# Kernel tuning notes

Measured on AMD Instinct MI355X. Metric: run time of the kernel, lower is better.

The kernel has to match this reference:

```python
import jax, jax.numpy as jnp
import numpy as np

NB_KERNEL = 16
NUM_POS_EMB = 16
DMAX = 20.0


def _grbf_encode(d):
    # d: (..., ) distances; centers 0..DMAX in NB_KERNEL steps (matches torch.arange(0, 20*(1+1/15), 20/15))
    centers = jnp.linspace(0.0, DMAX, NB_KERNEL, dtype=jnp.float32)
    return jnp.exp(-jnp.square(d[..., None] - centers))


def _positional_embeddings(d):
    # d: (..., ) float offsets
    freq = jnp.exp(jnp.arange(0, NUM_POS_EMB, 2, dtype=jnp.float32) * (-(np.log(10000.0) / NUM_POS_EMB)))
    angles = d[..., None] * freq  # (..., NUM_POS_EMB//2)
    return jnp.concatenate([jnp.cos(angles), jnp.sin(angles)], axis=-1)


def setup_inputs() -> dict:
    key = jax.random.key(0)
    # coordinates in Angstrom-ish scale so pairwise distances span the RBF range
    crd = jax.random.normal(key, (4096, 4, 3), dtype=jnp.float32) * 10.0
    return {"crd": crd, "max_neigh": 64}


def reference(crd, max_neigh):
    nb_var = crd.shape[0]
    nb_neigh = min(max_neigh, nb_var - 1)

    # virtual Cbeta atom from backbone geometry
    b = crd[:, 1] - crd[:, 0]
    c = crd[:, 2] - crd[:, 1]
    a = jnp.cross(b, c)
    Cb = -0.58273431 * a + 0.56802827 * b - 0.54067466 * c + crd[:, 1]
    crd5 = jnp.concatenate([crd, Cb[:, None, :]], axis=1)  # (N, 5, 3)

    # pairwise CA distances, diagonal forced to -1 so self sorts first
    ca = crd5[:, 1]  # (N, 3)
    D = jnp.linalg.norm(ca[:, None, :] - ca[None, :, :], axis=-1)  # (N, N)
    diag = jnp.arange(nb_var)
    D = D.at[diag, diag].set(-1.0)

    # nb_neigh smallest distances (= top_k of -D); self is column 0
    neg_d, idx_pairs = jax.lax.top_k(-D, nb_neigh)  # (N, K)
    d = -neg_d
    d = d.at[:, 0].set(0.0)
    d = jnp.nan_to_num(d, nan=0.0)

    # all-pairs atom distances between residue i (5 atoms) and each neighbor j (5 atoms)
    neigh = crd5[idx_pairs]  # (N, K, 5, 3)
    diff = crd5[:, None, :, None, :] - neigh[:, :, None, :, :]  # (N, K, 5, 5, 3); [i,k,a,b]=crd[i,a]-crd[j,b]
    dist = jnp.linalg.norm(diff, axis=-1).reshape(nb_var, nb_neigh, 25)
    dist = _grbf_encode(dist).reshape(nb_var, nb_neigh, 25 * NB_KERNEL)
    dist = jnp.nan_to_num(dist, nan=0.0)

    # sinusoidal encoding of sequence-index offsets
    offsets = jnp.abs(diag[:, None] - idx_pairs).astype(jnp.float32)  # (N, K)
    pos = _positional_embeddings(offsets)  # (N, K, NUM_POS_EMB)

    return (d, dist, pos, idx_pairs)
```

## Files before the change

### kernel.cpp

```cpp
#include <hip/hip_runtime.h>
#include <math.h>

#define NBV 4096
#define KNE 64
#define D_OFF    0
#define DIST_OFF (NBV*KNE)
#define POS_OFF  (DIST_OFF + NBV*KNE*400)
#define IDX_OFF  (POS_OFF + NBV*KNE*16)

#define WS_CRD5 0
#define WS_CA4  (NBV*16)
#define WS_FLOATS (NBV*16 + NBV*4)

typedef float f4v __attribute__((ext_vector_type(4)));

__device__ __forceinline__ unsigned int f2sort(float f) {
  unsigned int u = __float_as_uint(f);
  return (u & 0x80000000u) ? ~u : (u | 0x80000000u);
}
__device__ __forceinline__ float sort2f(unsigned int s) {
  unsigned int u = (s & 0x80000000u) ? (s & 0x7FFFFFFFu) : ~s;
  return __uint_as_float(u);
}

__device__ __forceinline__ float4 crd5_f4(const float* __restrict__ crd, int r,
                                          int q) {
  if (q < 3) return ((const float4*)crd)[r * 3 + q];
  const float4 a = ((const float4*)crd)[r * 3 + 0];
  const float4 b = ((const float4*)crd)[r * 3 + 1];
  const float4 c = ((const float4*)crd)[r * 3 + 2];
  const float bx = a.w - a.x, by = b.x - a.y, bz = b.y - a.z;
  const float cx = b.z - a.w, cy = b.w - b.x, cz = c.x - b.y;
  const float axv = by * cz - bz * cy;
  const float ayv = bz * cx - bx * cz;
  const float azv = bx * cy - by * cx;
  return make_float4(
      -0.58273431f * axv + 0.56802827f * bx - 0.54067466f * cx + a.w,
      -0.58273431f * ayv + 0.56802827f * by - 0.54067466f * cy + b.x,
      -0.58273431f * azv + 0.56802827f * bz - 0.54067466f * cz + b.y, 0.0f);
}

__global__ __launch_bounds__(256) void prep_k(const float* __restrict__ crd,
                                              float* __restrict__ ws) {
  const int r = blockIdx.x * 256 + threadIdx.x;
  const float4 a = ((const float4*)crd)[r * 3 + 0];
  const float4 b = ((const float4*)crd)[r * 3 + 1];
  const float4 c = ((const float4*)crd)[r * 3 + 2];
  const float bx = a.w - a.x, by = b.x - a.y, bz = b.y - a.z;
  const float cx = b.z - a.w, cy = b.w - b.x, cz = c.x - b.y;
  const float axv = by * cz - bz * cy;
  const float ayv = bz * cx - bx * cz;
  const float azv = bx * cy - by * cx;
  const float cbx = -0.58273431f * axv + 0.56802827f * bx - 0.54067466f * cx + a.w;
  const float cby = -0.58273431f * ayv + 0.56802827f * by - 0.54067466f * cy + b.x;
  const float cbz = -0.58273431f * azv + 0.56802827f * bz - 0.54067466f * cz + b.y;

  float4* row = (float4*)(ws + WS_CRD5 + r * 16);
  row[0] = a;
  row[1] = b;
  row[2] = c;
  row[3] = make_float4(cbx, cby, cbz, 0.0f);
  ((float4*)(ws + WS_CA4))[r] = make_float4(a.w, b.x, b.y, 0.0f);
}

template <bool USE_WS>
__global__ __launch_bounds__(256) void fused_k(const float* __restrict__ crd,
                                               const float* __restrict__ ws,
                                               float* __restrict__ out) {
  const int i = blockIdx.x;
  const int t = threadIdx.x;

  __shared__ float region0[2688];
  __shared__ unsigned long long cand[512];
  __shared__ int jidx[64];
  __shared__ unsigned int cnt;
  __shared__ int selbin;
  __shared__ unsigned int wsum[4];

  unsigned int* hist = (unsigned int*)region0;
  float* rows = region0;
  float* dvals = region0 + 1040;

  for (int b = t; b < 2048; b += 256) hist[b] = 0u;
  if (t == 0) cnt = 0u;
  __syncthreads();

  float cax, cay, caz;
  if (USE_WS) {
    const float4 c4 = ((const float4*)(ws + WS_CA4))[i];
    cax = c4.x; cay = c4.y; caz = c4.z;
  } else {
    cax = crd[i * 12 + 3]; cay = crd[i * 12 + 4]; caz = crd[i * 12 + 5];
  }

  float dv[16];
#pragma unroll
  for (int s = 0; s < 16; s++) {
    const int j = t + 256 * s;
    float jx, jy, jz;
    if (USE_WS) {
      const float4 c4 = ((const float4*)(ws + WS_CA4))[j];
      jx = c4.x; jy = c4.y; jz = c4.z;
    } else {
      jx = crd[j * 12 + 3]; jy = crd[j * 12 + 4]; jz = crd[j * 12 + 5];
    }
    const float dx = cax - jx, dy = cay - jy, dz = caz - jz;
    float f = sqrtf(dx * dx + dy * dy + dz * dz);
    if (j == i) f = -1.0f;
    dv[s] = f;
    int b = (int)(f * 16.0f);
    b = b < 0 ? 0 : (b > 2047 ? 2047 : b);
    atomicAdd(&hist[b], 1u);
  }
  __syncthreads();

  unsigned int bc[8];
  unsigned int loc = 0;
#pragma unroll
  for (int r = 0; r < 8; r++) { bc[r] = hist[t * 8 + r]; loc += bc[r]; }
  const int lane = t & 63, wid = t >> 6;
  unsigned int x = loc;
#pragma unroll
  for (int off = 1; off < 64; off <<= 1) {
    unsigned int y = __shfl_up(x, off, 64);
    if (lane >= off) x += y;
  }
  if (lane == 63) wsum[wid] = x;
  __syncthreads();
  unsigned int woff = 0;
#pragma unroll
  for (int w = 0; w < 4; w++)
    if (w < wid) woff += wsum[w];
  unsigned int c = woff + x - loc;
#pragma unroll
  for (int r = 0; r < 8; r++) {
    if (c < 64u && c + bc[r] >= 64u) selbin = t * 8 + r;
    c += bc[r];
  }
  __syncthreads();
  const int B = selbin;

#pragma unroll
  for (int s = 0; s < 16; s++) {
    const float f = dv[s];
    int b = (int)(f * 16.0f);
    b = b < 0 ? 0 : (b > 2047 ? 2047 : b);
    if (b <= B) {
      const unsigned int p = atomicAdd(&cnt, 1u);
      if (p < 512u) {
        const int j = t + 256 * s;
        cand[p] = (((unsigned long long)f2sort(f)) << 32) | (unsigned int)j;
      }
    }
  }
  __syncthreads();
  unsigned int M = cnt;
  if (M > 512u) M = 512u;
  for (int p = t; p < 512; p += 256)
    if ((unsigned)p >= M) cand[p] = 0xFFFFFFFFFFFFFFFFull;

  for (int ksz = 2; ksz <= 512; ksz <<= 1) {
    for (int jsz = ksz >> 1; jsz > 0; jsz >>= 1) {
      __syncthreads();
      const int a = ((t & ~(jsz - 1)) << 1) | (t & (jsz - 1));
      const int b2 = a | jsz;
      const unsigned long long va = cand[a], vb = cand[b2];
      const bool up = ((a & ksz) == 0);
      if ((va > vb) == up) { cand[a] = vb; cand[b2] = va; }
    }
  }
  __syncthreads();

  if (t < KNE) {
    const unsigned long long key = cand[t];
    const int j = (int)(unsigned int)(key & 0xFFFFFFFFull);
    const float f = sort2f((unsigned int)(key >> 32));
    jidx[t] = j;
    out[D_OFF + i * KNE + t] = (t == 0) ? 0.0f : f;
    out[IDX_OFF + i * KNE + t] = (float)j;

    const float freqs[8] = {1.0f, 0.31622776601683794f, 0.1f,
                            0.031622776601683791f, 0.01f,
                            0.0031622776601683794f, 0.001f,
                            0.00031622776601683794f};
    int di = i - j;
    if (di < 0) di = -di;
    const float offv = (float)di;
    float cc[8], ss[8];
#pragma unroll
    for (int q = 0; q < 8; q++) {
      const float ang = offv * freqs[q];
      ss[q] = sinf(ang);
      cc[q] = cosf(ang);
    }
    float4* pv = (float4*)(out + POS_OFF + (size_t)(i * KNE + t) * 16);
    pv[0] = make_float4(cc[0], cc[1], cc[2], cc[3]);
    pv[1] = make_float4(cc[4], cc[5], cc[6], cc[7]);
    pv[2] = make_float4(ss[0], ss[1], ss[2], ss[3]);
    pv[3] = make_float4(ss[4], ss[5], ss[6], ss[7]);
  }
  __syncthreads();

  {
    const int s = t >> 2, q = t & 3;
    float4 v;
    if (USE_WS) v = ((const float4*)ws)[jidx[s] * 4 + q];
    else        v = crd5_f4(crd, jidx[s], q);
    ((float4*)rows)[s * 4 + q] = v;
    if (t < 4) {
      float4 v2;
      if (USE_WS) v2 = ((const float4*)ws)[i * 4 + t];
      else        v2 = crd5_f4(crd, i, t);
      ((float4*)rows)[64 * 4 + t] = v2;
    }
  }
  __syncthreads();

#pragma unroll
  for (int it = 0; it < 7; it++) {
    const int pid = t + 256 * it;
    if (pid < 1600) {
      const int k = pid / 25;
      const int p = pid - k * 25;
      const int p0 = p / 5;
      const int p1 = p - p0 * 5;
      const float dx = rows[64 * 16 + p0 * 3 + 0] - rows[k * 16 + p1 * 3 + 0];
      const float dy = rows[64 * 16 + p0 * 3 + 1] - rows[k * 16 + p1 * 3 + 1];
      const float dz = rows[64 * 16 + p0 * 3 + 2] - rows[k * 16 + p1 * 3 + 2];
      dvals[pid] = sqrtf(dx * dx + dy * dy + dz * dz);
    }
  }
  __syncthreads();

  const float step = 20.0f / 15.0f;
  f4v* dst = (f4v*)(out + DIST_OFF) + (size_t)i * 6400;
#pragma unroll
  for (int s = 0; s < 25; s++) {
    const int f4i = t + 256 * s;
    const int pair = f4i >> 2;
    const float cb0 = (float)((f4i & 3) * 4) * step;
    const float f = dvals[pair];
    f4v o;
    float tt;
    tt = f - cb0;                 o.x = __expf(-(tt * tt));
    tt = f - (cb0 + step);        o.y = __expf(-(tt * tt));
    tt = f - (cb0 + 2.0f * step); o.z = __expf(-(tt * tt));
    tt = f - (cb0 + 3.0f * step); o.w = __expf(-(tt * tt));
    __builtin_nontemporal_store(o, dst + f4i);
  }
}

extern "C" void kernel_launch(void* const* d_in, const int* in_sizes, int n_in,
                              void* d_out, int out_size, void* d_ws, size_t ws_size,
                              hipStream_t stream) {
  const float* crd = (const float*)d_in[0];
  float* out = (float*)d_out;
  if (ws_size >= (size_t)WS_FLOATS * sizeof(float)) {
    float* ws = (float*)d_ws;
    hipLaunchKernelGGL(prep_k, dim3(NBV / 256), dim3(256), 0, stream, crd, ws);
    hipLaunchKernelGGL(fused_k<true>, dim3(NBV), dim3(256), 0, stream, crd, ws,
                       out);
  } else {
    hipLaunchKernelGGL(fused_k<false>, dim3(NBV), dim3(256), 0, stream, crd,
                       (const float*)nullptr, out);
  }
}
```

Baseline: 457.4 us.

## Shrink bitonic sort, spread pos-emb across threads, use recurrence for RBF exps

The bitonic sort now runs only over the next power of two at or above the candidate count (at least 64) rather than always 512, which removes sort stages. The positional embedding is split across all 256 threads with sincosf and nontemporal stores instead of 64 threads each writing 16 values, and the coordinate loads are issued before that work to overlap latency. The Gaussian RBF computes one exp per group of four centers and gets the rest by multiplying with a geometric ratio, cutting the exp count from four to two. The recurrence with a clamp and rounded constants may shift results slightly in float precision.

```diff
diff --git a/kernel.cpp b/kernel.cpp
--- a/kernel.cpp
+++ b/kernel.cpp
@@ -159,14 +159,18 @@
   for (int p = t; p < 512; p += 256)
     if ((unsigned)p >= M) cand[p] = 0xFFFFFFFFFFFFFFFFull;
 
-  for (int ksz = 2; ksz <= 512; ksz <<= 1) {
+  int P = 64;
+  while (P < (int)M) P <<= 1;
+  for (int ksz = 2; ksz <= P; ksz <<= 1) {
     for (int jsz = ksz >> 1; jsz > 0; jsz >>= 1) {
       __syncthreads();
-      const int a = ((t & ~(jsz - 1)) << 1) | (t & (jsz - 1));
-      const int b2 = a | jsz;
-      const unsigned long long va = cand[a], vb = cand[b2];
-      const bool up = ((a & ksz) == 0);
-      if ((va > vb) == up) { cand[a] = vb; cand[b2] = va; }
+      if (t < (P >> 1)) {
+        const int a = ((t & ~(jsz - 1)) << 1) | (t & (jsz - 1));
+        const int b2 = a | jsz;
+        const unsigned long long va = cand[a], vb = cand[b2];
+        const bool up = ((a & ksz) == 0);
+        if ((va > vb) == up) { cand[a] = vb; cand[b2] = va; }
+      }
     }
   }
   __syncthreads();
@@ -178,42 +182,43 @@
     jidx[t] = j;
     out[D_OFF + i * KNE + t] = (t == 0) ? 0.0f : f;
     out[IDX_OFF + i * KNE + t] = (float)j;
-
-    const float freqs[8] = {1.0f, 0.31622776601683794f, 0.1f,
-                            0.031622776601683791f, 0.01f,
-                            0.0031622776601683794f, 0.001f,
-                            0.00031622776601683794f};
+  }
+  __syncthreads();
+
+  const int sr = t >> 2, qq = t & 3;
+  float4 v, v2;
+  if (USE_WS) v = ((const float4*)ws)[jidx[sr] * 4 + qq];
+  else        v = crd5_f4(crd, jidx[sr], qq);
+  if (t < 4) {
+    if (USE_WS) v2 = ((const float4*)ws)[i * 4 + t];
+    else        v2 = crd5_f4(crd, i, t);
+  }
+
+  {
+    const int n = sr, g = qq;
+    const int j = jidx[n];
     int di = i - j;
     if (di < 0) di = -di;
     const float offv = (float)di;
-    float cc[8], ss[8];
-#pragma unroll
-    for (int q = 0; q < 8; q++) {
-      const float ang = offv * freqs[q];
-      ss[q] = sinf(ang);
-      cc[q] = cosf(ang);
-    }
-    float4* pv = (float4*)(out + POS_OFF + (size_t)(i * KNE + t) * 16);
-    pv[0] = make_float4(cc[0], cc[1], cc[2], cc[3]);
-    pv[1] = make_float4(cc[4], cc[5], cc[6], cc[7]);
-    pv[2] = make_float4(ss[0], ss[1], ss[2], ss[3]);
-    pv[3] = make_float4(ss[4], ss[5], ss[6], ss[7]);
-  }
-  __syncthreads();
-
-  {
-    const int s = t >> 2, q = t & 3;
-    float4 v;
-    if (USE_WS) v = ((const float4*)ws)[jidx[s] * 4 + q];
-    else        v = crd5_f4(crd, jidx[s], q);
-    ((float4*)rows)[s * 4 + q] = v;
-    if (t < 4) {
-      float4 v2;
-      if (USE_WS) v2 = ((const float4*)ws)[i * 4 + t];
-      else        v2 = crd5_f4(crd, i, t);
-      ((float4*)rows)[64 * 4 + t] = v2;
-    }
-  }
+    const bool hi = (g & 1);
+    const float fA = hi ? 0.01f                   : 1.0f;
+    const float fB = hi ? 0.0031622776601683794f  : 0.31622776601683794f;
+    const float fC = hi ? 0.001f                  : 0.1f;
+    const float fD = hi ? 0.00031622776601683794f : 0.031622776601683791f;
+    float s0, c0, s1, c1, s2, c2, s3, c3;
+    sincosf(offv * fA, &s0, &c0);
+    sincosf(offv * fB, &s1, &c1);
+    sincosf(offv * fC, &s2, &c2);
+    sincosf(offv * fD, &s3, &c3);
+    f4v o;
+    if (g < 2) o = (f4v){c0, c1, c2, c3};
+    else       o = (f4v){s0, s1, s2, s3};
+    f4v* pv = (f4v*)(out + POS_OFF) + (size_t)(i * KNE + n) * 4 + g;
+    __builtin_nontemporal_store(o, pv);
+  }
+
+  ((float4*)rows)[sr * 4 + qq] = v;
+  if (t < 4) ((float4*)rows)[64 * 4 + t] = v2;
   __syncthreads();
 
 #pragma unroll
@@ -233,19 +238,24 @@
   __syncthreads();
 
   const float step = 20.0f / 15.0f;
+  const float TWO_S = 2.6666667f;
+  const float S2 = 1.7777778f;
+  const float RHO = 0.02856550f;
   f4v* dst = (f4v*)(out + DIST_OFF) + (size_t)i * 6400;
 #pragma unroll
   for (int s = 0; s < 25; s++) {
     const int f4i = t + 256 * s;
     const int pair = f4i >> 2;
     const float cb0 = (float)((f4i & 3) * 4) * step;
-    const float f = dvals[pair];
+    float u = dvals[pair] - cb0;
+    u = fminf(u, 16.0f);
+    float e = __expf(-u * u);
+    float q = __expf(fmaf(TWO_S, u, -S2));
     f4v o;
-    float tt;
-    tt = f - cb0;                 o.x = __expf(-(tt * tt));
-    tt = f - (cb0 + step);        o.y = __expf(-(tt * tt));
-    tt = f - (cb0 + 2.0f * step); o.z = __expf(-(tt * tt));
-    tt = f - (cb0 + 3.0f * step); o.w = __expf(-(tt * tt));
+    o.x = e;
+    e *= q;           o.y = e;
+    q *= RHO; e *= q; o.z = e;
+    q *= RHO; e *= q; o.w = e;
     __builtin_nontemporal_store(o, dst + f4i);
   }
 }
```

Result: faster. 448.1 us (-2.0%).
